# Optimization experiments

Hardware: AMD Instinct MI355X
Metric: run time of the kernel (lower is better)

Reference implementation:

```python
import jax, jax.numpy as jnp
from jax import lax
import numpy as np

B, T, NCLS, D = 64, 2048, 20, 2048
LCS_LEN, FSD_LEN = 64, 32
LAMB1, LAMB2, LAMB3 = 1.0, 5e-5, 8e-5
LAMB_LCS, LAMB_FSD = 0.01, 0.01
FEAT_MARGIN = 50.0
THRES = 0.5
GAMMA = 0.1


def cos_sim(a, b):
    a = a / jnp.linalg.norm(a, axis=1, keepdims=True)
    b = b / jnp.linalg.norm(b, axis=1, keepdims=True)
    return a @ b.T


def dp_fsd(c0, c1):
    # soft-LCS/DTW-style recurrence with maxGamma (soft max) over 3 neighbors
    h = c0.shape[-1] // 2
    m = cos_sim(c0[:, :h], c1[:, :h])  # [L, L]
    g = cos_sim(c0[:, h:], c1[:, h:])  # [L, L]
    L = m.shape[0]

    def row_step(prev_row, mg):
        m_row, g_row = mg
        diag = prev_row[:-1]  # C[i-1, j-1]
        up = prev_row[1:]     # C[i-1, j]

        def col_step(left, xs):  # left = C[i, j-1]
            d, u, mij, gij = xs
            neigh = jnp.stack([d, gij + u, gij + left])
            val = mij + GAMMA * jax.nn.logsumexp(neigh / GAMMA)
            return val, val

        _, row_vals = lax.scan(col_step, jnp.zeros((), m.dtype), (diag, up, m_row, g_row))
        new_row = jnp.concatenate([jnp.zeros((1,), m.dtype), row_vals])
        return new_row, None

    final_row, _ = lax.scan(row_step, jnp.zeros(L + 1, m.dtype), (m, g))
    return final_row[-1]


def dp_lcs(c0, c1):
    s = cos_sim(c0, c1)  # [L, L]
    L = s.shape[0]

    def row_step(prev_row, s_row):
        diag = prev_row[:-1]
        up = prev_row[1:]

        def col_step(left, xs):
            d, u, sij = xs
            val = jnp.where(sij > THRES, d + sij, jnp.maximum(u, left))
            return val, val

        _, row_vals = lax.scan(col_step, jnp.zeros((), s.dtype), (diag, up, s_row))
        return jnp.concatenate([jnp.zeros((1,), s.dtype), row_vals]), None

    final_row, _ = lax.scan(row_step, jnp.zeros(L + 1, s.dtype), s)
    return final_row[-1]


def cls_criterion(p, lab):
    return -jnp.mean(jnp.sum(jnp.log(p + 1e-10) * lab, axis=1))


def forward_once(ai_cls, ac_cls, ab_cls, vlab, att, ai_feat, ac_feat, ab_feat, ai_cas):
    bs = ai_cls.shape[0]
    ones = jnp.ones((bs, 1), ai_cls.dtype)
    zeros = jnp.zeros((bs, 1), ai_cls.dtype)
    inst_lab = jnp.concatenate([vlab, zeros], axis=1)
    cont_lab = jnp.concatenate([vlab, ones], axis=1)
    back_lab = jnp.concatenate([jnp.zeros_like(vlab), ones], axis=1)
    inst_lab = inst_lab / jnp.sum(inst_lab, axis=1, keepdims=True)
    cont_lab = cont_lab / jnp.sum(cont_lab, axis=1, keepdims=True)
    back_lab = back_lab / jnp.sum(back_lab, axis=1, keepdims=True)

    inst_loss = cls_criterion(ai_cls, inst_lab)
    cont_loss = cls_criterion(ac_cls, cont_lab)
    back_loss = cls_criterion(ab_cls, back_lab)

    guide_loss = jnp.mean(jnp.sum(jnp.abs(1.0 - ai_cas[:, :, -1] - lax.stop_gradient(att[:, :, 0])), axis=1))

    n_inst = jnp.linalg.norm(ai_feat, axis=1)
    n_cont = jnp.linalg.norm(ac_feat, axis=1)
    n_back = jnp.linalg.norm(ab_feat, axis=1)
    f1 = jnp.maximum(FEAT_MARGIN - n_inst + n_cont, 0.0)
    f2 = jnp.maximum(FEAT_MARGIN - n_cont + n_back, 0.0)
    f3 = n_back
    feat_loss = jnp.mean((f1 + f2 + f3) ** 2)

    sparse_loss = jnp.mean(jnp.sum(att[:, :, :2], axis=1))

    cls_loss = inst_loss + cont_loss + back_loss  # THUMOS14 weights 1/1/1
    return cls_loss + LAMB1 * guide_loss + LAMB2 * feat_loss + LAMB3 * sparse_loss


def _pair_loss(vals, pair_label):
    bs = vals.shape[0]
    pos = jnp.sum(vals * pair_label)
    neg = jnp.sum(vals * (1.0 - pair_label))
    pos_num = jnp.sum(pair_label)
    neg_num = bs - pos_num
    return neg / (neg_num + 1e-10) - pos / (pos_num + 1e-10)


def ftcl_forward(act_inst_cls_0, act_cont_cls_0, act_back_cls_0, vid_label_0, temp_att_0,
                 act_inst_feat_0, act_cont_feat_0, act_back_feat_0, act_inst_cas_0,
                 lcs_candi_0, fsd_act_candi_0, fsd_bak_candi_0,
                 act_inst_cls_1, act_cont_cls_1, act_back_cls_1, vid_label_1, temp_att_1,
                 act_inst_feat_1, act_cont_feat_1, act_back_feat_1, act_inst_cas_1,
                 lcs_candi_1, fsd_act_candi_1, fsd_bak_candi_1):
    loss_0 = forward_once(act_inst_cls_0, act_cont_cls_0, act_back_cls_0, vid_label_0, temp_att_0,
                          act_inst_feat_0, act_cont_feat_0, act_back_feat_0, act_inst_cas_0)
    loss_1 = forward_once(act_inst_cls_1, act_cont_cls_1, act_back_cls_1, vid_label_1, temp_att_1,
                          act_inst_feat_1, act_cont_feat_1, act_back_feat_1, act_inst_cas_1)
    acm_loss = (loss_0 + loss_1) / 2.0

    pair_label = (jnp.sum(vid_label_0 * vid_label_1, axis=1) > 0).astype(jnp.float32)  # [B]

    lcs = jax.vmap(dp_lcs)(lcs_candi_0, lcs_candi_1)  # [B]
    lcs_loss = _pair_loss(lcs, pair_label)

    # pair==1 -> act_1, pair==0 -> bak_1 (matches the per-sample branch in torch)
    fsd_c1 = jnp.where(pair_label[:, None, None] > 0, fsd_act_candi_1, fsd_bak_candi_1)
    fsd = jax.vmap(dp_fsd)(fsd_act_candi_0, fsd_c1)  # [B]
    fsd_loss = _pair_loss(fsd, pair_label)

    return acm_loss + LAMB_LCS * lcs_loss + LAMB_FSD * fsd_loss


def setup_inputs() -> dict:
    key = jax.random.key(0)
    ks = iter(jax.random.split(key, 32))
    rand = lambda s: jax.random.uniform(next(ks), s, jnp.float32)
    randn = lambda s: jax.random.normal(next(ks), s, jnp.float32)
    inp = {}
    for sfx in ('0', '1'):
        inp[f'act_inst_cls_{sfx}'] = rand((B, NCLS + 1))
        inp[f'act_cont_cls_{sfx}'] = rand((B, NCLS + 1))
        inp[f'act_back_cls_{sfx}'] = rand((B, NCLS + 1))
        inp[f'vid_label_{sfx}'] = jnp.ones((B, NCLS), jnp.float32)
        inp[f'temp_att_{sfx}'] = rand((B, T, 3))
        inp[f'act_inst_feat_{sfx}'] = randn((B, D))
        inp[f'act_cont_feat_{sfx}'] = randn((B, D))
        inp[f'act_back_feat_{sfx}'] = randn((B, D))
        inp[f'act_inst_cas_{sfx}'] = rand((B, T, NCLS + 1))
        inp[f'lcs_candi_{sfx}'] = randn((B, LCS_LEN, D))
        inp[f'fsd_act_candi_{sfx}'] = randn((B, FSD_LEN, D))
        inp[f'fsd_bak_candi_{sfx}'] = randn((B, FSD_LEN, D))
    return inp


def reference(act_inst_cls_0, act_cont_cls_0, act_back_cls_0, vid_label_0, temp_att_0,
              act_inst_feat_0, act_cont_feat_0, act_back_feat_0, act_inst_cas_0,
              lcs_candi_0, fsd_act_candi_0, fsd_bak_candi_0,
              act_inst_cls_1, act_cont_cls_1, act_back_cls_1, vid_label_1, temp_att_1,
              act_inst_feat_1, act_cont_feat_1, act_back_feat_1, act_inst_cas_1,
              lcs_candi_1, fsd_act_candi_1, fsd_bak_candi_1):
    return ftcl_forward(act_inst_cls_0, act_cont_cls_0, act_back_cls_0, vid_label_0, temp_att_0,
                        act_inst_feat_0, act_cont_feat_0, act_back_feat_0, act_inst_cas_0,
                        lcs_candi_0, fsd_act_candi_0, fsd_bak_candi_0,
                        act_inst_cls_1, act_cont_cls_1, act_back_cls_1, vid_label_1, temp_att_1,
                        act_inst_feat_1, act_cont_feat_1, act_back_feat_1, act_inst_cas_1,
                        lcs_candi_1, fsd_act_candi_1, fsd_bak_candi_1)
```

## Files before the change

### kernel.cpp

```cpp
#include <hip/hip_runtime.h>
#include <math.h>

#define Bn 64
#define Tn 2048
#define NCLS 20
#define Dn 2048
#define LCSL 64
#define FSDL 32

typedef __bf16 bf16x4 __attribute__((ext_vector_type(4)));
typedef __bf16 bf16x8 __attribute__((ext_vector_type(8)));
typedef float f32x4 __attribute__((ext_vector_type(4)));

#define WS_LCS 0
#define WS_FSD 64
#define WS_NORM 128
#define WS_GS 512

#define AUXB 176
#define NBLK 304

__global__ __launch_bounds__(512) void mega_kernel(
    const float* __restrict__ lcs0, const float* __restrict__ lcs1,
    const float* __restrict__ fA0, const float* __restrict__ fA1,
    const float* __restrict__ fB1,
    const float* __restrict__ vid0, const float* __restrict__ vid1,
    const float* __restrict__ cas0, const float* __restrict__ att0,
    const float* __restrict__ cas1, const float* __restrict__ att1,
    const float* __restrict__ f0, const float* __restrict__ f1,
    const float* __restrict__ f2, const float* __restrict__ f3,
    const float* __restrict__ f4, const float* __restrict__ f5,
    float* __restrict__ ws) {
    __shared__ __align__(16) __bf16 tA[2][4096];
    __shared__ __align__(16) __bf16 tB[2][4096];
    __shared__ __align__(16) float S[64 * 68];
    __shared__ float inv[128];
    const int t = threadIdx.x;
    const int bid = blockIdx.x;
    const int w = t >> 6, lane = t & 63;
    const int quad = lane >> 4, l16 = lane & 15;

    if (bid < 128) {
        const int gb = bid;
        const int N = Bn * Tn;
        float g0 = 0.f, s0 = 0.f, g1 = 0.f, s1 = 0.f;
        for (int n = gb * 512 + t; n < 2 * N; n += 128 * 512) {
            int sfx = (n >= N);
            int m = sfx ? (n - N) : n;
            const float* cas = sfx ? cas1 : cas0;
            const float* att = sfx ? att1 : att0;
            float a0 = att[m * 3 + 0];
            float a1 = att[m * 3 + 1];
            float g = fabsf(1.0f - cas[m * (NCLS + 1) + NCLS] - a0);
            float s = a0 + a1;
            if (sfx) { g1 += g; s1 += s; } else { g0 += g; s0 += s; }
        }
        float* red = S;
        float vals[4] = {g0, s0, g1, s1};
        #pragma unroll
        for (int v = 0; v < 4; ++v) red[v * 512 + t] = vals[v];
        __syncthreads();
        for (int o = 256; o; o >>= 1) {
            if (t < o) {
                #pragma unroll
                for (int v = 0; v < 4; ++v) red[v * 512 + t] += red[v * 512 + t + o];
            }
            __syncthreads();
        }
        if (t < 4) ws[WS_GS + gb * 4 + t] = red[t * 512];
    } else if (bid < AUXB) {
        int R = (bid - 128) * 8 + w;
        const float* arr[6] = {f0, f1, f2, f3, f4, f5};
        const float* p = arr[R >> 6] + (size_t)(R & 63) * Dn;
        float s = 0.f;
        #pragma unroll
        for (int qd = 0; qd < 8; ++qd) {
            float4 v = *(const float4*)(p + qd * 256 + lane * 4);
            s += v.x * v.x + v.y * v.y + v.z * v.z + v.w * v.w;
        }
        for (int off = 32; off; off >>= 1) s += __shfl_down(s, off);
        if (lane == 0) ws[WS_NORM + R] = sqrtf(s);
    } else if (bid < 240) {
        const int b = bid - AUXB;
        const float* c0 = lcs0 + (size_t)b * LCSL * Dn;
        const float* c1 = lcs1 + (size_t)b * LCSL * Dn;
        constexpr int KC = 32;

        f32x4 acc[2] = {};
        float sqa[2] = {0.f, 0.f}, sqb[2] = {0.f, 0.f};
        float4 pA[2], pB[2];

        auto LOADL = [&](int st) {
            #pragma unroll
            for (int l = 0; l < 2; ++l) {
                int idx4 = l * 512 + t;
                int row = idx4 >> 4, kq4 = idx4 & 15;
                pA[l] = *(const float4*)(c0 + (size_t)row * Dn + st * 64 + kq4 * 4);
                pB[l] = *(const float4*)(c1 + (size_t)row * Dn + st * 64 + kq4 * 4);
            }
        };
        auto WRITEL = [&](int buf) {
            #pragma unroll
            for (int l = 0; l < 2; ++l) {
                int idx4 = l * 512 + t;
                int row = idx4 >> 4, kq4 = idx4 & 15;
                int c = kq4 >> 1, h = kq4 & 1;
                int pos = row * 64 + ((c ^ (row & 7)) << 3) + h * 4;
                float4 av = pA[l], bv = pB[l];
                bf16x4 a4 = {(__bf16)av.x, (__bf16)av.y, (__bf16)av.z, (__bf16)av.w};
                bf16x4 b4 = {(__bf16)bv.x, (__bf16)bv.y, (__bf16)bv.z, (__bf16)bv.w};
                *(bf16x4*)&tA[buf][pos] = a4;
                *(bf16x4*)&tB[buf][pos] = b4;
                sqa[l] += av.x * av.x + av.y * av.y + av.z * av.z + av.w * av.w;
                sqb[l] += bv.x * bv.x + bv.y * bv.y + bv.z * bv.z + bv.w * bv.w;
            }
        };

        LOADL(0);
        WRITEL(0);
        LOADL(1);
        __syncthreads();
        for (int kc = 0; kc < KC; ++kc) {
            const int cur = kc & 1;
            #pragma unroll
            for (int s = 0; s < 2; ++s) {
                int ar = (w >> 1) * 16 + l16;
                int ac_ = (s * 4 + quad) ^ (ar & 7);
                bf16x8 af = *(const bf16x8*)&tA[cur][ar * 64 + (ac_ << 3)];
                #pragma unroll
                for (int tj = 0; tj < 2; ++tj) {
                    int br = (w & 1) * 32 + tj * 16 + l16;
                    int bc = (s * 4 + quad) ^ (br & 7);
                    bf16x8 bf = *(const bf16x8*)&tB[cur][br * 64 + (bc << 3)];
                    acc[tj] = __builtin_amdgcn_mfma_f32_16x16x32_bf16(af, bf, acc[tj], 0, 0, 0);
                }
            }
            if (kc + 1 < KC) {
                WRITEL(cur ^ 1);
                if (kc + 2 < KC) LOADL(kc + 2);
                __syncthreads();
            }
        }
        #pragma unroll
        for (int l = 0; l < 2; ++l) {
            float sa = sqa[l], sb = sqb[l];
            #pragma unroll
            for (int m = 1; m < 16; m <<= 1) {
                sa += __shfl_xor(sa, m);
                sb += __shfl_xor(sb, m);
            }
            if ((t & 15) == 0) {
                int r = l * 32 + (t >> 4);
                inv[r] = sa;
                inv[64 + r] = sb;
            }
        }
        __syncthreads();
        if (t < 128) inv[t] = 1.0f / sqrtf(inv[t]);
        __syncthreads();
        #pragma unroll
        for (int tj = 0; tj < 2; ++tj)
            #pragma unroll
            for (int rg = 0; rg < 4; ++rg) {
                int row = (w >> 1) * 16 + quad * 4 + rg;
                int col = (w & 1) * 32 + tj * 16 + l16;
                S[row * 68 + col] = acc[tj][rg] * inv[row] * inv[64 + col];
            }
        __syncthreads();
        if (t < 64) {
            float prev = 0.f, prevprev = 0.f;
            float sval_next = S[t * 68 + 0];
            for (int d = 2; d <= 128; ++d) {
                float s = sval_next;
                int jn = d - t - 1;
                if (jn >= 0 && jn < 64) sval_next = S[t * 68 + jn];
                float up = __shfl_up(prev, 1);
                float dg = __shfl_up(prevprev, 1);
                if (t == 0) { up = 0.f; dg = 0.f; }
                int j = d - t - 1;
                float left = prev;
                float val = (s > 0.5f) ? (dg + s) : fmaxf(up, left);
                float cur = (j >= 1 && j <= 64) ? val : 0.f;
                prevprev = prev;
                prev = cur;
            }
            if (t == 63) ws[WS_LCS + b] = prev;
        }
    } else {
        const int b = bid - 240;
        float ps = 0.f;
        for (int c = 0; c < NCLS; ++c) ps += vid0[b * NCLS + c] * vid1[b * NCLS + c];
        const float* base1 = (ps > 0.f) ? fA1 : fB1;
        const float* c0 = fA0 + (size_t)b * FSDL * Dn;
        const float* c1 = base1 + (size_t)b * FSDL * Dn;
        const int wi = w >> 1, wj = w & 1;
        float* Ml = S;
        float* Gl = S + 1152;
        constexpr int KC = 16;

        for (int ph = 0; ph < 2; ++ph) {
            const int off = ph * 1024;
            f32x4 acc = {};
            float sqa = 0.f, sqb = 0.f;
            float4 pA, pB;
            auto LOADF = [&](int st) {
                int row = t >> 4, kq4 = t & 15;
                pA = *(const float4*)(c0 + (size_t)row * Dn + off + st * 64 + kq4 * 4);
                pB = *(const float4*)(c1 + (size_t)row * Dn + off + st * 64 + kq4 * 4);
            };
            auto WRITEF = [&](int buf) {
                int row = t >> 4, kq4 = t & 15;
                int c = kq4 >> 1, h = kq4 & 1;
                int pos = row * 64 + ((c ^ (row & 7)) << 3) + h * 4;
                float4 av = pA, bv = pB;
                bf16x4 a4 = {(__bf16)av.x, (__bf16)av.y, (__bf16)av.z, (__bf16)av.w};
                bf16x4 b4 = {(__bf16)bv.x, (__bf16)bv.y, (__bf16)bv.z, (__bf16)bv.w};
                *(bf16x4*)&tA[buf][pos] = a4;
                *(bf16x4*)&tB[buf][pos] = b4;
                sqa += av.x * av.x + av.y * av.y + av.z * av.z + av.w * av.w;
                sqb += bv.x * bv.x + bv.y * bv.y + bv.z * bv.z + bv.w * bv.w;
            };

            LOADF(0);
            WRITEF(0);
            LOADF(1);
            __syncthreads();
            for (int kc = 0; kc < KC; ++kc) {
                const int cur = kc & 1;
                if (w < 4) {
                    #pragma unroll
                    for (int s = 0; s < 2; ++s) {
                        int ar = wi * 16 + l16;
                        int ac_ = (s * 4 + quad) ^ (ar & 7);
                        bf16x8 af = *(const bf16x8*)&tA[cur][ar * 64 + (ac_ << 3)];
                        int br = wj * 16 + l16;
                        int bc = (s * 4 + quad) ^ (br & 7);
                        bf16x8 bf = *(const bf16x8*)&tB[cur][br * 64 + (bc << 3)];
                        acc = __builtin_amdgcn_mfma_f32_16x16x32_bf16(af, bf, acc, 0, 0, 0);
                    }
                }
                if (kc + 1 < KC) {
                    WRITEF(cur ^ 1);
                    if (kc + 2 < KC) LOADF(kc + 2);
                    __syncthreads();
                }
            }
            {
                float sa = sqa, sb = sqb;
                #pragma unroll
                for (int m = 1; m < 16; m <<= 1) {
                    sa += __shfl_xor(sa, m);
                    sb += __shfl_xor(sb, m);
                }
                if ((t & 15) == 0) {
                    int r = t >> 4;
                    inv[r] = sa;
                    inv[32 + r] = sb;
                }
            }
            __syncthreads();
            if (t < 64) inv[t] = 1.0f / sqrtf(inv[t]);
            __syncthreads();
            if (w < 4) {
                float* T = (ph == 0) ? Ml : Gl;
                #pragma unroll
                for (int rg = 0; rg < 4; ++rg) {
                    int row = wi * 16 + quad * 4 + rg;
                    int col = wj * 16 + l16;
                    T[row * 36 + col] = acc[rg] * inv[row] * inv[32 + col];
                }
            }
            __syncthreads();
        }
        if (t < 32) {
            float prev = 0.f, prevprev = 0.f;
            float m_next = Ml[t * 36 + 0], g_next = Gl[t * 36 + 0];
            for (int d = 2; d <= 64; ++d) {
                float m = m_next, g = g_next;
                int jn = d - t - 1;
                if (jn >= 0 && jn < 32) { m_next = Ml[t * 36 + jn]; g_next = Gl[t * 36 + jn]; }
                float up = __shfl_up(prev, 1);
                float dg = __shfl_up(prevprev, 1);
                if (t == 0) { up = 0.f; dg = 0.f; }
                int j = d - t - 1;
                float left = prev;
                float x0 = dg * 10.0f;
                float x1 = (g + up) * 10.0f;
                float x2 = (g + left) * 10.0f;
                float mx = fmaxf(x0, fmaxf(x1, x2));
                float lse = mx + __logf(__expf(x0 - mx) + __expf(x1 - mx) + __expf(x2 - mx));
                float val = m + 0.1f * lse;
                float cur = (j >= 1 && j <= 32) ? val : 0.f;
                prevprev = prev;
                prev = cur;
            }
            if (t == 31) ws[WS_FSD + b] = prev;
        }
    }
}

__device__ __forceinline__ float4 wbr4(float4 v, float4* redw, int t) {
    #pragma unroll
    for (int m = 1; m < 64; m <<= 1) {
        v.x += __shfl_xor(v.x, m);
        v.y += __shfl_xor(v.y, m);
        v.z += __shfl_xor(v.z, m);
        v.w += __shfl_xor(v.w, m);
    }
    if ((t & 63) == 0) redw[t >> 6] = v;
    __syncthreads();
    float4 r;
    r.x = redw[0].x + redw[1].x + redw[2].x + redw[3].x;
    r.y = redw[0].y + redw[1].y + redw[2].y + redw[3].y;
    r.z = redw[0].z + redw[1].z + redw[2].z + redw[3].z;
    r.w = redw[0].w + redw[1].w + redw[2].w + redw[3].w;
    __syncthreads();
    return r;
}

__global__ __launch_bounds__(256) void final_kernel(
    const float* __restrict__ ai0, const float* __restrict__ ac0,
    const float* __restrict__ ab0, const float* __restrict__ vid0,
    const float* __restrict__ ai1, const float* __restrict__ ac1,
    const float* __restrict__ ab1, const float* __restrict__ vid1,
    const float* __restrict__ ws, float* __restrict__ out) {
    __shared__ float rs0[Bn], rs1[Bn], plsh[Bn];
    __shared__ __align__(16) float4 redw[4];
    int t = threadIdx.x;
    if (t < Bn) {
        float s0 = 0.f, s1 = 0.f, pp = 0.f;
        for (int c = 0; c < NCLS; ++c) {
            float a = vid0[t * NCLS + c], bl = vid1[t * NCLS + c];
            s0 += a; s1 += bl; pp += a * bl;
        }
        rs0[t] = s0;
        rs1[t] = s1;
        plsh[t] = (pp > 0.f) ? 1.f : 0.f;
    }
    __syncthreads();

    float inst0 = 0.f, cont0 = 0.f, back0 = 0.f;
    float inst1 = 0.f, cont1 = 0.f, back1 = 0.f;
    for (int idx = t; idx < Bn * (NCLS + 1); idx += 256) {
        int b = idx / (NCLS + 1), c = idx % (NCLS + 1);
        float v0 = (c < NCLS) ? vid0[b * NCLS + c] : 0.f;
        float v1 = (c < NCLS) ? vid1[b * NCLS + c] : 0.f;
        float wI0 = (c < NCLS) ? (v0 / rs0[b]) : 0.f;
        float wC0 = ((c < NCLS) ? v0 : 1.f) / (rs0[b] + 1.f);
        float wI1 = (c < NCLS) ? (v1 / rs1[b]) : 0.f;
        float wC1 = ((c < NCLS) ? v1 : 1.f) / (rs1[b] + 1.f);
        inst0 += logf(ai0[idx] + 1e-10f) * wI0;
        cont0 += logf(ac0[idx] + 1e-10f) * wC0;
        inst1 += logf(ai1[idx] + 1e-10f) * wI1;
        cont1 += logf(ac1[idx] + 1e-10f) * wC1;
        if (c == NCLS) {
            back0 += logf(ab0[idx] + 1e-10f);
            back1 += logf(ab1[idx] + 1e-10f);
        }
    }

    float g0 = 0.f, s0v = 0.f, g1 = 0.f, s1v = 0.f;
    if (t < 128) {
        float4 g = *(const float4*)&ws[WS_GS + t * 4];
        g0 = g.x; s0v = g.y; g1 = g.z; s1v = g.w;
    }

    float fv0 = 0.f, fv1 = 0.f;
    if (t < Bn) {
        const float* nm = ws + WS_NORM;
        {
            float ni = nm[0 * Bn + t], nc = nm[1 * Bn + t], nb = nm[2 * Bn + t];
            float f1 = fmaxf(50.0f - ni + nc, 0.f);
            float f2 = fmaxf(50.0f - nc + nb, 0.f);
            float f = f1 + f2 + nb;
            fv0 = f * f;
        }
        {
            float ni = nm[3 * Bn + t], nc = nm[4 * Bn + t], nb = nm[5 * Bn + t];
            float f1 = fmaxf(50.0f - ni + nc, 0.f);
            float f2 = fmaxf(50.0f - nc + nb, 0.f);
            float f = f1 + f2 + nb;
            fv1 = f * f;
        }
    }

    float posL = 0.f, negL = 0.f, posF = 0.f, negF = 0.f, pln = 0.f;
    if (t < Bn) {
        float pl = plsh[t];
        float lv = ws[WS_LCS + t];
        float fv = ws[WS_FSD + t];
        posL = lv * pl; negL = lv * (1.f - pl);
        posF = fv * pl; negF = fv * (1.f - pl);
        pln = pl;
    }

    float4 r1 = wbr4({inst0, cont0, back0, inst1}, redw, t);
    float4 r2 = wbr4({cont1, back1, g0, s0v}, redw, t);
    float4 r3 = wbr4({g1, s1v, fv0, fv1}, redw, t);
    float4 r4 = wbr4({posL, negL, posF, negF}, redw, t);
    float4 r5 = wbr4({pln, 0.f, 0.f, 0.f}, redw, t);

    if (t == 0) {
        float cls0 = -(r1.x + r1.y + r1.z) / (float)Bn;
        float cls1 = -(r1.w + r2.x + r2.y) / (float)Bn;
        float guide0 = r2.z / (float)Bn;
        float sparse0 = r2.w / (float)(Bn * 2);
        float guide1 = r3.x / (float)Bn;
        float sparse1 = r3.y / (float)(Bn * 2);
        float sFeat0 = r3.z / (float)Bn;
        float sFeat1 = r3.w / (float)Bn;
        float loss0 = cls0 + 1.0f * guide0 + 5e-05f * sFeat0 + 8e-05f * sparse0;
        float loss1 = cls1 + 1.0f * guide1 + 5e-05f * sFeat1 + 8e-05f * sparse1;
        float acm = 0.5f * (loss0 + loss1);
        float posn = r5.x;
        float negn = (float)Bn - posn;
        float lcs_loss = r4.y / (negn + 1e-10f) - r4.x / (posn + 1e-10f);
        float fsd_loss = r4.w / (negn + 1e-10f) - r4.z / (posn + 1e-10f);
        out[0] = acm + 0.01f * lcs_loss + 0.01f * fsd_loss;
    }
}

extern "C" void kernel_launch(void* const* d_in, const int* in_sizes, int n_in,
                              void* d_out, int out_size, void* d_ws, size_t ws_size,
                              hipStream_t stream) {
    (void)in_sizes; (void)n_in; (void)out_size; (void)ws_size;
    const float* ai0  = (const float*)d_in[0];
    const float* ac0  = (const float*)d_in[1];
    const float* ab0  = (const float*)d_in[2];
    const float* vid0 = (const float*)d_in[3];
    const float* att0 = (const float*)d_in[4];
    const float* fi0  = (const float*)d_in[5];
    const float* fc0  = (const float*)d_in[6];
    const float* fb0  = (const float*)d_in[7];
    const float* cas0 = (const float*)d_in[8];
    const float* lcs0 = (const float*)d_in[9];
    const float* fsdA0 = (const float*)d_in[10];
    const float* ai1  = (const float*)d_in[12];
    const float* ac1  = (const float*)d_in[13];
    const float* ab1  = (const float*)d_in[14];
    const float* vid1 = (const float*)d_in[15];
    const float* att1 = (const float*)d_in[16];
    const float* fi1  = (const float*)d_in[17];
    const float* fc1  = (const float*)d_in[18];
    const float* fb1  = (const float*)d_in[19];
    const float* cas1 = (const float*)d_in[20];
    const float* lcs1 = (const float*)d_in[21];
    const float* fsdA1 = (const float*)d_in[22];
    const float* fsdB1 = (const float*)d_in[23];

    float* ws = (float*)d_ws;

    mega_kernel<<<NBLK, 512, 0, stream>>>(
        lcs0, lcs1, fsdA0, fsdA1, fsdB1, vid0, vid1, cas0, att0, cas1, att1,
        fi0, fc0, fb0, fi1, fc1, fb1, ws);
    final_kernel<<<1, 256, 0, stream>>>(ai0, ac0, ab0, vid0, ai1, ac1, ab1, vid1,
                                        ws, (float*)d_out);
}
```

Measured before the change: 227.1 us.

## Reorder block roles so heavy LCS/FSD blocks launch first; fuse FSD halves across waves

Block IDs are reassigned so the 64 LCS GEMM+DP blocks and 64 FSD blocks are dispatched first, ahead of the reduction and norm blocks. This lets the long-latency blocks start early while the lighter blocks fill in behind them. The FSD path no longer runs the two feature halves in sequence with only 4 of 8 waves active. Instead, all 8 waves work at once, each half handled by 4 waves, with both halves loaded together per stage. This halves the FSD loop iterations and barriers but doubles register buffers per thread.

```diff
diff --git a/kernel.cpp b/kernel.cpp
--- a/kernel.cpp
+++ b/kernel.cpp
@@ -17,7 +17,6 @@
 #define WS_NORM 128
 #define WS_GS 512
 
-#define AUXB 176
 #define NBLK 304
 
 __global__ __launch_bounds__(512) void mega_kernel(
@@ -40,48 +39,8 @@
     const int w = t >> 6, lane = t & 63;
     const int quad = lane >> 4, l16 = lane & 15;
 
-    if (bid < 128) {
-        const int gb = bid;
-        const int N = Bn * Tn;
-        float g0 = 0.f, s0 = 0.f, g1 = 0.f, s1 = 0.f;
-        for (int n = gb * 512 + t; n < 2 * N; n += 128 * 512) {
-            int sfx = (n >= N);
-            int m = sfx ? (n - N) : n;
-            const float* cas = sfx ? cas1 : cas0;
-            const float* att = sfx ? att1 : att0;
-            float a0 = att[m * 3 + 0];
-            float a1 = att[m * 3 + 1];
-            float g = fabsf(1.0f - cas[m * (NCLS + 1) + NCLS] - a0);
-            float s = a0 + a1;
-            if (sfx) { g1 += g; s1 += s; } else { g0 += g; s0 += s; }
-        }
-        float* red = S;
-        float vals[4] = {g0, s0, g1, s1};
-        #pragma unroll
-        for (int v = 0; v < 4; ++v) red[v * 512 + t] = vals[v];
-        __syncthreads();
-        for (int o = 256; o; o >>= 1) {
-            if (t < o) {
-                #pragma unroll
-                for (int v = 0; v < 4; ++v) red[v * 512 + t] += red[v * 512 + t + o];
-            }
-            __syncthreads();
-        }
-        if (t < 4) ws[WS_GS + gb * 4 + t] = red[t * 512];
-    } else if (bid < AUXB) {
-        int R = (bid - 128) * 8 + w;
-        const float* arr[6] = {f0, f1, f2, f3, f4, f5};
-        const float* p = arr[R >> 6] + (size_t)(R & 63) * Dn;
-        float s = 0.f;
-        #pragma unroll
-        for (int qd = 0; qd < 8; ++qd) {
-            float4 v = *(const float4*)(p + qd * 256 + lane * 4);
-            s += v.x * v.x + v.y * v.y + v.z * v.z + v.w * v.w;
-        }
-        for (int off = 32; off; off >>= 1) s += __shfl_down(s, off);
-        if (lane == 0) ws[WS_NORM + R] = sqrtf(s);
-    } else if (bid < 240) {
-        const int b = bid - AUXB;
+    if (bid < 64) {
+        const int b = bid;
         const float* c0 = lcs0 + (size_t)b * LCSL * Dn;
         const float* c1 = lcs1 + (size_t)b * LCSL * Dn;
         constexpr int KC = 32;
@@ -186,92 +145,98 @@
             }
             if (t == 63) ws[WS_LCS + b] = prev;
         }
-    } else {
-        const int b = bid - 240;
+    } else if (bid < 128) {
+        const int b = bid - 64;
         float ps = 0.f;
         for (int c = 0; c < NCLS; ++c) ps += vid0[b * NCLS + c] * vid1[b * NCLS + c];
         const float* base1 = (ps > 0.f) ? fA1 : fB1;
         const float* c0 = fA0 + (size_t)b * FSDL * Dn;
         const float* c1 = base1 + (size_t)b * FSDL * Dn;
-        const int wi = w >> 1, wj = w & 1;
+        const int h = w >> 2, wi = (w >> 1) & 1, wj = w & 1;
         float* Ml = S;
         float* Gl = S + 1152;
         constexpr int KC = 16;
 
-        for (int ph = 0; ph < 2; ++ph) {
-            const int off = ph * 1024;
-            f32x4 acc = {};
-            float sqa = 0.f, sqb = 0.f;
-            float4 pA, pB;
-            auto LOADF = [&](int st) {
-                int row = t >> 4, kq4 = t & 15;
-                pA = *(const float4*)(c0 + (size_t)row * Dn + off + st * 64 + kq4 * 4);
-                pB = *(const float4*)(c1 + (size_t)row * Dn + off + st * 64 + kq4 * 4);
-            };
-            auto WRITEF = [&](int buf) {
-                int row = t >> 4, kq4 = t & 15;
-                int c = kq4 >> 1, h = kq4 & 1;
-                int pos = row * 64 + ((c ^ (row & 7)) << 3) + h * 4;
-                float4 av = pA, bv = pB;
+        f32x4 acc = {};
+        float sqa[2] = {0.f, 0.f}, sqb[2] = {0.f, 0.f};
+        float4 pA[2], pB[2];
+
+        auto LOADF = [&](int st) {
+            #pragma unroll
+            for (int l = 0; l < 2; ++l) {
+                int idx4 = l * 512 + t;
+                int tr = idx4 >> 4, kq4 = idx4 & 15;
+                int row = tr & 31, hh = tr >> 5;
+                pA[l] = *(const float4*)(c0 + (size_t)row * Dn + hh * 1024 + st * 64 + kq4 * 4);
+                pB[l] = *(const float4*)(c1 + (size_t)row * Dn + hh * 1024 + st * 64 + kq4 * 4);
+            }
+        };
+        auto WRITEF = [&](int buf) {
+            #pragma unroll
+            for (int l = 0; l < 2; ++l) {
+                int idx4 = l * 512 + t;
+                int tr = idx4 >> 4, kq4 = idx4 & 15;
+                int c = kq4 >> 1, hb = kq4 & 1;
+                int pos = tr * 64 + ((c ^ (tr & 7)) << 3) + hb * 4;
+                float4 av = pA[l], bv = pB[l];
                 bf16x4 a4 = {(__bf16)av.x, (__bf16)av.y, (__bf16)av.z, (__bf16)av.w};
                 bf16x4 b4 = {(__bf16)bv.x, (__bf16)bv.y, (__bf16)bv.z, (__bf16)bv.w};
                 *(bf16x4*)&tA[buf][pos] = a4;
                 *(bf16x4*)&tB[buf][pos] = b4;
-                sqa += av.x * av.x + av.y * av.y + av.z * av.z + av.w * av.w;
-                sqb += bv.x * bv.x + bv.y * bv.y + bv.z * bv.z + bv.w * bv.w;
-            };
-
-            LOADF(0);
-            WRITEF(0);
-            LOADF(1);
-            __syncthreads();
-            for (int kc = 0; kc < KC; ++kc) {
-                const int cur = kc & 1;
-                if (w < 4) {
-                    #pragma unroll
-                    for (int s = 0; s < 2; ++s) {
-                        int ar = wi * 16 + l16;
-                        int ac_ = (s * 4 + quad) ^ (ar & 7);
-                        bf16x8 af = *(const bf16x8*)&tA[cur][ar * 64 + (ac_ << 3)];
-                        int br = wj * 16 + l16;
-                        int bc = (s * 4 + quad) ^ (br & 7);
-                        bf16x8 bf = *(const bf16x8*)&tB[cur][br * 64 + (bc << 3)];
-                        acc = __builtin_amdgcn_mfma_f32_16x16x32_bf16(af, bf, acc, 0, 0, 0);
-                    }
-                }
-                if (kc + 1 < KC) {
-                    WRITEF(cur ^ 1);
-                    if (kc + 2 < KC) LOADF(kc + 2);
-                    __syncthreads();
-                }
-            }
-            {
-                float sa = sqa, sb = sqb;
-                #pragma unroll
-                for (int m = 1; m < 16; m <<= 1) {
-                    sa += __shfl_xor(sa, m);
-                    sb += __shfl_xor(sb, m);
-                }
-                if ((t & 15) == 0) {
-                    int r = t >> 4;
-                    inv[r] = sa;
-                    inv[32 + r] = sb;
-                }
-            }
-            __syncthreads();
-            if (t < 64) inv[t] = 1.0f / sqrtf(inv[t]);
-            __syncthreads();
-            if (w < 4) {
-                float* T = (ph == 0) ? Ml : Gl;
-                #pragma unroll
-                for (int rg = 0; rg < 4; ++rg) {
-                    int row = wi * 16 + quad * 4 + rg;
-                    int col = wj * 16 + l16;
-                    T[row * 36 + col] = acc[rg] * inv[row] * inv[32 + col];
-                }
-            }
-            __syncthreads();
-        }
+                sqa[l] += av.x * av.x + av.y * av.y + av.z * av.z + av.w * av.w;
+                sqb[l] += bv.x * bv.x + bv.y * bv.y + bv.z * bv.z + bv.w * bv.w;
+            }
+        };
+
+        LOADF(0);
+        WRITEF(0);
+        LOADF(1);
+        __syncthreads();
+        for (int kc = 0; kc < KC; ++kc) {
+            const int cur = kc & 1;
+            #pragma unroll
+            for (int s = 0; s < 2; ++s) {
+                int ar = h * 32 + wi * 16 + l16;
+                int ac_ = (s * 4 + quad) ^ (ar & 7);
+                bf16x8 af = *(const bf16x8*)&tA[cur][ar * 64 + (ac_ << 3)];
+                int br = h * 32 + wj * 16 + l16;
+                int bc = (s * 4 + quad) ^ (br & 7);
+                bf16x8 bf = *(const bf16x8*)&tB[cur][br * 64 + (bc << 3)];
+                acc = __builtin_amdgcn_mfma_f32_16x16x32_bf16(af, bf, acc, 0, 0, 0);
+            }
+            if (kc + 1 < KC) {
+                WRITEF(cur ^ 1);
+                if (kc + 2 < KC) LOADF(kc + 2);
+                __syncthreads();
+            }
+        }
+        #pragma unroll
+        for (int l = 0; l < 2; ++l) {
+            float sa = sqa[l], sb = sqb[l];
+            #pragma unroll
+            for (int m = 1; m < 16; m <<= 1) {
+                sa += __shfl_xor(sa, m);
+                sb += __shfl_xor(sb, m);
+            }
+            if ((t & 15) == 0) {
+                int r = l * 32 + (t >> 4);
+                inv[r] = sa;
+                inv[64 + r] = sb;
+            }
+        }
+        __syncthreads();
+        if (t < 128) inv[t] = 1.0f / sqrtf(inv[t]);
+        __syncthreads();
+        {
+            float* T = h ? Gl : Ml;
+            #pragma unroll
+            for (int rg = 0; rg < 4; ++rg) {
+                int row = wi * 16 + quad * 4 + rg;
+                int col = wj * 16 + l16;
+                T[row * 36 + col] = acc[rg] * inv[h * 32 + row] * inv[64 + h * 32 + col];
+            }
+        }
+        __syncthreads();
         if (t < 32) {
             float prev = 0.f, prevprev = 0.f;
             float m_next = Ml[t * 36 + 0], g_next = Gl[t * 36 + 0];
@@ -296,6 +261,46 @@
             }
             if (t == 31) ws[WS_FSD + b] = prev;
         }
+    } else if (bid < 256) {
+        const int gb = bid - 128;
+        const int N = Bn * Tn;
+        float g0 = 0.f, s0 = 0.f, g1 = 0.f, s1 = 0.f;
+        for (int n = gb * 512 + t; n < 2 * N; n += 128 * 512) {
+            int sfx = (n >= N);
+            int m = sfx ? (n - N) : n;
+            const float* cas = sfx ? cas1 : cas0;
+            const float* att = sfx ? att1 : att0;
+            float a0 = att[m * 3 + 0];
+            float a1 = att[m * 3 + 1];
+            float g = fabsf(1.0f - cas[m * (NCLS + 1) + NCLS] - a0);
+            float s = a0 + a1;
+            if (sfx) { g1 += g; s1 += s; } else { g0 += g; s0 += s; }
+        }
+        float* red = S;
+        float vals[4] = {g0, s0, g1, s1};
+        #pragma unroll
+        for (int v = 0; v < 4; ++v) red[v * 512 + t] = vals[v];
+        __syncthreads();
+        for (int o = 256; o; o >>= 1) {
+            if (t < o) {
+                #pragma unroll
+                for (int v = 0; v < 4; ++v) red[v * 512 + t] += red[v * 512 + t + o];
+            }
+            __syncthreads();
+        }
+        if (t < 4) ws[WS_GS + gb * 4 + t] = red[t * 512];
+    } else {
+        int R = (bid - 256) * 8 + w;
+        const float* arr[6] = {f0, f1, f2, f3, f4, f5};
+        const float* p = arr[R >> 6] + (size_t)(R & 63) * Dn;
+        float s = 0.f;
+        #pragma unroll
+        for (int qd = 0; qd < 8; ++qd) {
+            float4 v = *(const float4*)(p + qd * 256 + lane * 4);
+            s += v.x * v.x + v.y * v.y + v.z * v.z + v.w * v.w;
+        }
+        for (int off = 32; off; off >>= 1) s += __shfl_down(s, off);
+        if (lane == 0) ws[WS_NORM + R] = sqrtf(s);
     }
 }
 
```

New measurement: 230.3 us. No clear change (+1.4%).
